# Kernel tuning notes

Measured on AMD Instinct MI355X. Metric: run time of the kernel, lower is better.

## Reference

```python
import jax, jax.numpy as jnp
import numpy as np

D_MODEL = 1024
N_HEADS = 16
D_HEAD = D_MODEL // N_HEADS


def setup_inputs() -> dict:
    key = jax.random.key(0)
    k1, k2, k3 = jax.random.split(key, 3)
    B, N = 2, 2048
    x = jax.random.normal(k1, (B, N, D_MODEL), dtype=jnp.float32)
    # torch nn.Linear(d, 3d, bias=False): y = x @ W.T ; we store W_qkv as [D, 3D]
    scale_in = 1.0 / np.sqrt(D_MODEL)
    W_qkv = jax.random.uniform(k2, (D_MODEL, 3 * D_MODEL), dtype=jnp.float32,
                               minval=-scale_in, maxval=scale_in)
    W_out = jax.random.uniform(k3, (D_MODEL, D_MODEL), dtype=jnp.float32,
                               minval=-scale_in, maxval=scale_in)
    return {"x": x, "W_qkv": W_qkv, "W_out": W_out}


def reference(x, W_qkv, W_out):
    B, N, D = x.shape
    qkv = x @ W_qkv                                    # [B, N, 3D]
    q, k, v = jnp.split(qkv, 3, axis=-1)
    # [B, N, D] -> [B, H, N, d_head]
    def heads(t):
        return t.reshape(B, N, N_HEADS, D_HEAD).transpose(0, 2, 1, 3)
    q, k, v = heads(q), heads(k), heads(v)
    scores = jnp.einsum('bhnd,bhmd->bhnm', q, k) / np.sqrt(D_HEAD)  # [B,H,N,N]
    causal_mask = jnp.triu(jnp.ones((N, N), dtype=bool), k=1)
    scores = jnp.where(causal_mask, -jnp.inf, scores)
    attn = jax.nn.softmax(scores, axis=-1)             # [B,H,N,N]
    out = jnp.einsum('bhnm,bhmd->bhnd', attn, v)       # [B,H,N,d_head]
    out = out.transpose(0, 2, 1, 3).reshape(B, N, D)
    out = out @ W_out.T if False else out @ W_out      # W_out stored [D,D], x @ W
    return out, attn
```

## Files before the change

kernel.cpp:

```cpp
#include <hip/hip_runtime.h>
#include <hip/hip_bf16.h>

typedef __bf16 bf16;
typedef __bf16 bf16x4 __attribute__((ext_vector_type(4)));
typedef __bf16 bf16x8 __attribute__((ext_vector_type(8)));
typedef float  f32x4  __attribute__((ext_vector_type(4)));

#define MFMA16(a, b, c) __builtin_amdgcn_mfma_f32_16x16x32_bf16((a), (b), (c), 0, 0, 0)

typedef const __attribute__((address_space(1))) void* gptr_t;
typedef __attribute__((address_space(3))) void* sptr_t;

__device__ __forceinline__ void load_lds16(const bf16* g, bf16* l) {
  __builtin_amdgcn_global_load_lds((gptr_t)g, (sptr_t)l, 16, 0, 0);
}

__global__ __launch_bounds__(256) void detect_dtype(const unsigned short* __restrict__ w,
                                                    int* __restrict__ flag) {
  __shared__ int cnt[256];
  int c = 0;
#pragma unroll
  for (int k = 0; k < 16; ++k) {
    unsigned short v = w[(threadIdx.x * 16 + k) * 2];
    int e = (v >> 7) & 0xFF;
    c += (e >= 90 && e <= 130) ? 1 : 0;
  }
  cnt[threadIdx.x] = c;
  __syncthreads();
  if (threadIdx.x == 0) {
    int t = 0;
    for (int i = 0; i < 256; ++i) t += cnt[i];
    *flag = (t > 2048) ? 1 : 0;
  }
}

__global__ __launch_bounds__(256) void convert_to_bf16(const void* __restrict__ in,
                                                       bf16* __restrict__ out,
                                                       const int* __restrict__ flag) {
  const int i0 = (blockIdx.x * 256 + threadIdx.x) * 8;
  if (*flag) {
    *(bf16x8*)(out + i0) = *(const bf16x8*)((const bf16*)in + i0);
  } else {
    const float* p = (const float*)in;
    float4 a = *(const float4*)(p + i0);
    float4 b = *(const float4*)(p + i0 + 4);
    bf16x8 v;
    v[0] = (bf16)a.x; v[1] = (bf16)a.y; v[2] = (bf16)a.z; v[3] = (bf16)a.w;
    v[4] = (bf16)b.x; v[5] = (bf16)b.y; v[6] = (bf16)b.z; v[7] = (bf16)b.w;
    *(bf16x8*)(out + i0) = v;
  }
}

__global__ __launch_bounds__(256) void transpose_any(const void* __restrict__ in,
                                                     bf16* __restrict__ out,
                                                     const int* __restrict__ flag,
                                                     int R, int C) {
  __shared__ bf16 t[64][65];
  const int c0 = blockIdx.x * 64, r0 = blockIdx.y * 64;
  const int tid = threadIdx.x;
  const int lc = tid & 63, lr4 = tid >> 6;
  if (*flag) {
    const bf16* p = (const bf16*)in;
#pragma unroll
    for (int i = 0; i < 16; ++i) {
      int r = i * 4 + lr4;
      t[r][lc] = p[(size_t)(r0 + r) * C + c0 + lc];
    }
  } else {
    const float* p = (const float*)in;
#pragma unroll
    for (int i = 0; i < 16; ++i) {
      int r = i * 4 + lr4;
      t[r][lc] = (bf16)p[(size_t)(r0 + r) * C + c0 + lc];
    }
  }
  __syncthreads();
#pragma unroll
  for (int i = 0; i < 16; ++i) {
    int r = i * 4 + lr4;
    out[(size_t)(c0 + r) * R + r0 + lc] = t[lc][r];
  }
}

__global__ __launch_bounds__(256) void transpose_v(const bf16* __restrict__ qkv,
                                                   bf16* __restrict__ vt) {
  __shared__ bf16 t[64][65];
  const int bh = blockIdx.y, b = bh >> 4, h = bh & 15;
  const int j0 = blockIdx.x * 64;
  const int tid = threadIdx.x;
  const int lc = tid & 63, lr4 = tid >> 6;
  const bf16* src = qkv + (size_t)b * 2048 * 3072 + 2048 + (size_t)h * 64;
#pragma unroll
  for (int i = 0; i < 16; ++i) {
    int j = i * 4 + lr4;
    t[j][lc] = src[(size_t)(j0 + j) * 3072 + lc];
  }
  __syncthreads();
  bf16* dst = vt + (size_t)bh * 64 * 2048;
#pragma unroll
  for (int i = 0; i < 16; ++i) {
    int d = i * 4 + lr4;
    dst[(size_t)d * 2048 + j0 + lc] = t[lc][d];
  }
}

template <typename CT>
__global__ __launch_bounds__(256) void gemm_bt(const bf16* __restrict__ A,
                                               const bf16* __restrict__ Bt,
                                               CT* __restrict__ C,
                                               int K, int ldc) {
  __shared__ bf16 a_lds[128 * 32];
  __shared__ bf16 b_lds[128 * 32];
  const int tid = threadIdx.x;
  const int w = tid >> 6, lane = tid & 63, l15 = lane & 15, quad = lane >> 4;
  const int wr = w >> 1, wc = w & 1;
  const int m0 = blockIdx.y * 128, n0 = blockIdx.x * 128;

  const f32x4 fz = {0.f, 0.f, 0.f, 0.f};
  f32x4 acc[4][4];
#pragma unroll
  for (int i = 0; i < 4; ++i)
#pragma unroll
    for (int j = 0; j < 4; ++j) acc[i][j] = fz;

  for (int k0 = 0; k0 < K; k0 += 32) {
#pragma unroll
    for (int i = 0; i < 2; ++i) {
      int c = tid + i * 256;
      int r = c >> 2, kk = c & 3;
      load_lds16(A + (size_t)(m0 + r) * K + k0 + kk * 8, &a_lds[c * 8]);
      load_lds16(Bt + (size_t)(n0 + r) * K + k0 + kk * 8, &b_lds[c * 8]);
    }
    __syncthreads();
    bf16x8 af[4], bfr[4];
#pragma unroll
    for (int mb = 0; mb < 4; ++mb)
      af[mb] = *(const bf16x8*)&a_lds[(wr * 64 + mb * 16 + l15) * 32 + quad * 8];
#pragma unroll
    for (int nb = 0; nb < 4; ++nb)
      bfr[nb] = *(const bf16x8*)&b_lds[(wc * 64 + nb * 16 + l15) * 32 + quad * 8];
#pragma unroll
    for (int mb = 0; mb < 4; ++mb)
#pragma unroll
      for (int nb = 0; nb < 4; ++nb)
        acc[mb][nb] = MFMA16(af[mb], bfr[nb], acc[mb][nb]);
    __syncthreads();
  }

#pragma unroll
  for (int mb = 0; mb < 4; ++mb)
#pragma unroll
    for (int nb = 0; nb < 4; ++nb) {
      int row = m0 + wr * 64 + mb * 16 + quad * 4;
      int col = n0 + wc * 64 + nb * 16 + l15;
#pragma unroll
      for (int r = 0; r < 4; ++r)
        C[(size_t)(row + r) * ldc + col] = (CT)acc[mb][nb][r];
    }
}

__device__ __forceinline__ void compute_st(const bf16* k_lds, const bf16x8 (&qf)[2][2],
                                           int l15, int quad, f32x4 (&st)[8][2]) {
  const f32x4 fz = {0.f, 0.f, 0.f, 0.f};
  __builtin_amdgcn_s_setprio(1);
#pragma unroll
  for (int jb = 0; jb < 8; ++jb) {
    const int jl = jb * 16 + l15;
    const char* kb = (const char*)k_lds + jl * 128;
    const int sw = (jl & 7) << 4;
    bf16x8 kf0 = *(const bf16x8*)(kb + ((quad * 16) ^ sw));
    bf16x8 kf1 = *(const bf16x8*)(kb + ((64 + quad * 16) ^ sw));
    st[jb][0] = MFMA16(kf0, qf[0][0], fz);
    st[jb][0] = MFMA16(kf1, qf[0][1], st[jb][0]);
    st[jb][1] = MFMA16(kf0, qf[1][0], fz);
    st[jb][1] = MFMA16(kf1, qf[1][1], st[jb][1]);
  }
  __builtin_amdgcn_s_setprio(0);
}

__global__ __launch_bounds__(256) void fused_attn(const bf16* __restrict__ qkv,
                                                  const bf16* __restrict__ vt,
                                                  float* __restrict__ attn,
                                                  bf16* __restrict__ o_ws) {
  __shared__ bf16 k_lds[2][128 * 64];
  __shared__ bf16 vt_lds[64 * 128];
  __shared__ bf16 p_lds[128 * 128];

  const int bh = blockIdx.y;
  const int b = bh >> 4, h = bh & 15;
  const int qt = (bh & 16) ? (15 - (int)blockIdx.x) : (int)blockIdx.x;
  const int tid = threadIdx.x;
  const int w = tid >> 6, lane = tid & 63, l15 = lane & 15, quad = lane >> 4;
  const int q0 = qt * 128;

  const char* qkvb = (const char*)qkv;
  const size_t kbyte0 = ((size_t)b * 2048 * 3072 + 1024 + (size_t)h * 64) * 2;
  const size_t vtbyte0 = ((size_t)bh * 64) * 2048 * 2;

  bf16x8 qf[2][2];
#pragma unroll
  for (int ib = 0; ib < 2; ++ib)
#pragma unroll
    for (int ks = 0; ks < 2; ++ks) {
      const bf16* qp = qkv + ((size_t)b * 2048 + q0 + w * 32 + ib * 16 + l15) * 3072
                       + h * 64 + ks * 32 + quad * 8;
      bf16x8 v = *(const bf16x8*)qp;
      bf16x8 sv;
#pragma unroll
      for (int u = 0; u < 8; ++u) sv[u] = (bf16)((float)v[u] * 0.125f);
      qf[ib][ks] = sv;
    }

  float m_run[2] = {-3e38f, -3e38f};
  float l_run[2] = {0.f, 0.f};

  auto stage_k = [&](int kt, int buf) {
#pragma unroll
    for (int c = 0; c < 4; ++c) {
      const int L = c * 4096 + tid * 16;
      const int j = L >> 7, cb = L & 127;
      const char* src = qkvb + kbyte0 + (size_t)(kt * 128 + j) * 6144 + (cb ^ ((j & 7) << 4));
      load_lds16((const bf16*)src, (bf16*)((char*)k_lds[buf] + L));
    }
  };
  auto stage_v = [&](int kt) {
#pragma unroll
    for (int c = 0; c < 4; ++c) {
      const int L = c * 4096 + tid * 16;
      const int d = L >> 8, cb = L & 255;
      const char* src = (const char*)vt + vtbyte0 + (size_t)d * 4096 + kt * 256 + (cb ^ ((d & 7) << 4));
      load_lds16((const bf16*)src, (bf16*)((char*)vt_lds + L));
    }
  };

  stage_k(0, 0);
  __syncthreads();
  for (int kt = 0; kt <= qt; ++kt) {
    if (kt < qt) stage_k(kt + 1, (kt + 1) & 1);

    f32x4 st[8][2];
    compute_st(k_lds[kt & 1], qf, l15, quad, st);

    const bool diag = (kt == qt);
#pragma unroll
    for (int ib = 0; ib < 2; ++ib) {
      const int ig = q0 + w * 32 + ib * 16 + l15;
      float tmax = -3e38f;
#pragma unroll
      for (int jb = 0; jb < 8; ++jb)
#pragma unroll
        for (int r = 0; r < 4; ++r) {
          const int jg = kt * 128 + jb * 16 + quad * 4 + r;
          float s = st[jb][ib][r];
          if (diag && jg > ig) { s = -3e38f; st[jb][ib][r] = s; }
          tmax = fmaxf(tmax, s);
        }
      tmax = fmaxf(tmax, __shfl_xor(tmax, 16));
      tmax = fmaxf(tmax, __shfl_xor(tmax, 32));
      const float mnew = fmaxf(m_run[ib], tmax);
      float tsum = 0.f;
#pragma unroll
      for (int jb = 0; jb < 8; ++jb)
#pragma unroll
        for (int r = 0; r < 4; ++r) {
          const float s = st[jb][ib][r];
          tsum += (s > -1e38f) ? __expf(s - mnew) : 0.f;
        }
      tsum += __shfl_xor(tsum, 16);
      tsum += __shfl_xor(tsum, 32);
      l_run[ib] = l_run[ib] * __expf(m_run[ib] - mnew) + tsum;
      m_run[ib] = mnew;
    }
    __syncthreads();
  }

  const float invl[2] = {1.f / l_run[0], 1.f / l_run[1]};

  f32x4 oacc[2][4];
#pragma unroll
  for (int ib = 0; ib < 2; ++ib)
#pragma unroll
    for (int db = 0; db < 4; ++db) {
      const f32x4 fz = {0.f, 0.f, 0.f, 0.f};
      oacc[ib][db] = fz;
    }

  stage_k(0, 0);
  __syncthreads();
  for (int kt = 0; kt <= qt; ++kt) {
    if (kt < qt) stage_k(kt + 1, (kt + 1) & 1);
    stage_v(kt);

    f32x4 st[8][2];
    compute_st(k_lds[kt & 1], qf, l15, quad, st);

    const bool diag = (kt == qt);
#pragma unroll
    for (int ib = 0; ib < 2; ++ib) {
      const int ig = q0 + w * 32 + ib * 16 + l15;
      const int il = w * 32 + ib * 16 + l15;
#pragma unroll
      for (int jb = 0; jb < 8; ++jb) {
        bf16x4 pk;
#pragma unroll
        for (int r = 0; r < 4; ++r) {
          const int jg = kt * 128 + jb * 16 + quad * 4 + r;
          float p = __expf(st[jb][ib][r] - m_run[ib]) * invl[ib];
          if (diag && jg > ig) p = 0.f;
          pk[r] = (bf16)p;
        }
        *(bf16x4*)((char*)p_lds + il * 256 + ((jb * 32 + quad * 8) ^ ((il & 7) << 4))) = pk;
      }
    }
    __syncthreads();

    {
      float* abase = attn + ((size_t)bh << 22) + (size_t)q0 * 2048 + kt * 128;
#pragma unroll
      for (int it = 0; it < 16; ++it) {
        const int il = it * 8 + w * 2 + (lane >> 5);
        const int jb4 = (lane & 31) * 8;
        bf16x4 pv = *(const bf16x4*)((char*)p_lds + il * 256 + (jb4 ^ ((il & 7) << 4)));
        float4 f = {(float)pv[0], (float)pv[1], (float)pv[2], (float)pv[3]};
        *(float4*)(abase + (size_t)il * 2048 + (lane & 31) * 4) = f;
      }
    }

    __builtin_amdgcn_s_setprio(1);
#pragma unroll
    for (int js = 0; js < 4; ++js) {
      bf16x8 pa[2], vb[4];
#pragma unroll
      for (int ib = 0; ib < 2; ++ib) {
        const int il = w * 32 + ib * 16 + l15;
        pa[ib] = *(const bf16x8*)((char*)p_lds + il * 256 + ((js * 64 + quad * 16) ^ ((il & 7) << 4)));
      }
#pragma unroll
      for (int db = 0; db < 4; ++db) {
        const int dl = db * 16 + l15;
        vb[db] = *(const bf16x8*)((char*)vt_lds + dl * 256 + ((js * 64 + quad * 16) ^ ((dl & 7) << 4)));
      }
#pragma unroll
      for (int ib = 0; ib < 2; ++ib)
#pragma unroll
        for (int db = 0; db < 4; ++db)
          oacc[ib][db] = MFMA16(pa[ib], vb[db], oacc[ib][db]);
    }
    __builtin_amdgcn_s_setprio(0);
    __syncthreads();
  }

  for (int kt = qt + 1; kt < 16; ++kt) {
    float* abase = attn + ((size_t)bh << 22) + (size_t)q0 * 2048 + kt * 128;
    const float4 z4 = {0.f, 0.f, 0.f, 0.f};
#pragma unroll
    for (int it = 0; it < 16; ++it) {
      const int il = it * 8 + w * 2 + (lane >> 5);
      *(float4*)(abase + (size_t)il * 2048 + (lane & 31) * 4) = z4;
    }
  }

#pragma unroll
  for (int ib = 0; ib < 2; ++ib)
#pragma unroll
    for (int db = 0; db < 4; ++db)
#pragma unroll
      for (int r = 0; r < 4; ++r) {
        const int ig = q0 + w * 32 + ib * 16 + quad * 4 + r;
        const int dg = h * 64 + db * 16 + l15;
        o_ws[((size_t)b * 2048 + ig) * 1024 + dg] = (bf16)oacc[ib][db][r];
      }
}

extern "C" void kernel_launch(void* const* d_in, const int* in_sizes, int n_in,
                              void* d_out, int out_size, void* d_ws, size_t ws_size,
                              hipStream_t stream) {
  const void* x_raw = d_in[0];
  const void* w_qkv = d_in[1];
  const void* w_out = d_in[2];
  float* out  = (float*)d_out;
  float* attn = out + 4194304;

  bf16* ws     = (bf16*)d_ws;
  bf16* qkv_ws = ws;
  bf16* x_bf   = ws + 12582912;
  bf16* vt_ws  = ws + 12582912;
  bf16* woT    = ws + 12582912;
  bf16* wqkvT  = ws + 16777216;
  bf16* o_ws   = ws + 16777216;
  int*  flag   = (int*)(ws + 20971520);

  detect_dtype<<<1, 256, 0, stream>>>((const unsigned short*)w_qkv, flag);
  convert_to_bf16<<<2048, 256, 0, stream>>>(x_raw, x_bf, flag);
  transpose_any<<<dim3(48, 16), 256, 0, stream>>>(w_qkv, wqkvT, flag, 1024, 3072);
  gemm_bt<bf16><<<dim3(24, 32), 256, 0, stream>>>(x_bf, wqkvT, qkv_ws, 1024, 3072);
  transpose_v<<<dim3(32, 32), 256, 0, stream>>>(qkv_ws, vt_ws);
  fused_attn<<<dim3(16, 32), 256, 0, stream>>>(qkv_ws, vt_ws, attn, o_ws);
  transpose_any<<<dim3(16, 16), 256, 0, stream>>>(w_out, woT, flag, 1024, 1024);
  gemm_bt<float><<<dim3(8, 32), 256, 0, stream>>>(o_ws, woT, out, 1024, 1024);
}
```

Before: 694.7 us.

## Read K and V fragments directly from global memory, drop LDS staging and barriers

```diff
diff --git a/kernel.cpp b/kernel.cpp
--- a/kernel.cpp
+++ b/kernel.cpp
@@ -159,17 +159,15 @@
     }
 }
 
-__device__ __forceinline__ void compute_st(const bf16* k_lds, const bf16x8 (&qf)[2][2],
-                                           int l15, int quad, f32x4 (&st)[8][2]) {
+__device__ __forceinline__ void qk_tile(const char* kt_base, const bf16x8 (&qf)[2][2],
+                                        int l15, int quad, f32x4 (&st)[8][2]) {
   const f32x4 fz = {0.f, 0.f, 0.f, 0.f};
   __builtin_amdgcn_s_setprio(1);
 #pragma unroll
   for (int jb = 0; jb < 8; ++jb) {
-    const int jl = jb * 16 + l15;
-    const char* kb = (const char*)k_lds + jl * 128;
-    const int sw = (jl & 7) << 4;
-    bf16x8 kf0 = *(const bf16x8*)(kb + ((quad * 16) ^ sw));
-    bf16x8 kf1 = *(const bf16x8*)(kb + ((64 + quad * 16) ^ sw));
+    const char* kr = kt_base + (size_t)(jb * 16 + l15) * 6144 + quad * 16;
+    bf16x8 kf0 = *(const bf16x8*)kr;
+    bf16x8 kf1 = *(const bf16x8*)(kr + 64);
     st[jb][0] = MFMA16(kf0, qf[0][0], fz);
     st[jb][0] = MFMA16(kf1, qf[0][1], st[jb][0]);
     st[jb][1] = MFMA16(kf0, qf[1][0], fz);
@@ -178,12 +176,10 @@
   __builtin_amdgcn_s_setprio(0);
 }
 
-__global__ __launch_bounds__(256) void fused_attn(const bf16* __restrict__ qkv,
-                                                  const bf16* __restrict__ vt,
-                                                  float* __restrict__ attn,
-                                                  bf16* __restrict__ o_ws) {
-  __shared__ bf16 k_lds[2][128 * 64];
-  __shared__ bf16 vt_lds[64 * 128];
+__global__ __launch_bounds__(256, 2) void fused_attn(const bf16* __restrict__ qkv,
+                                                     const bf16* __restrict__ vt,
+                                                     float* __restrict__ attn,
+                                                     bf16* __restrict__ o_ws) {
   __shared__ bf16 p_lds[128 * 128];
 
   const int bh = blockIdx.y;
@@ -195,7 +191,17 @@
 
   const char* qkvb = (const char*)qkv;
   const size_t kbyte0 = ((size_t)b * 2048 * 3072 + 1024 + (size_t)h * 64) * 2;
-  const size_t vtbyte0 = ((size_t)bh * 64) * 2048 * 2;
+  const char* vtb = (const char*)vt + ((size_t)bh * 64) * 2048 * 2;
+
+  for (int kt = qt + 1; kt < 16; ++kt) {
+    float* abase = attn + ((size_t)bh << 22) + (size_t)q0 * 2048 + kt * 128;
+    const f32x4 z4 = {0.f, 0.f, 0.f, 0.f};
+#pragma unroll
+    for (int it = 0; it < 16; ++it) {
+      const int il = it * 8 + w * 2 + (lane >> 5);
+      __builtin_nontemporal_store(z4, (f32x4*)(abase + (size_t)il * 2048 + (lane & 31) * 4));
+    }
+  }
 
   bf16x8 qf[2][2];
 #pragma unroll
@@ -214,32 +220,9 @@
   float m_run[2] = {-3e38f, -3e38f};
   float l_run[2] = {0.f, 0.f};
 
-  auto stage_k = [&](int kt, int buf) {
-#pragma unroll
-    for (int c = 0; c < 4; ++c) {
-      const int L = c * 4096 + tid * 16;
-      const int j = L >> 7, cb = L & 127;
-      const char* src = qkvb + kbyte0 + (size_t)(kt * 128 + j) * 6144 + (cb ^ ((j & 7) << 4));
-      load_lds16((const bf16*)src, (bf16*)((char*)k_lds[buf] + L));
-    }
-  };
-  auto stage_v = [&](int kt) {
-#pragma unroll
-    for (int c = 0; c < 4; ++c) {
-      const int L = c * 4096 + tid * 16;
-      const int d = L >> 8, cb = L & 255;
-      const char* src = (const char*)vt + vtbyte0 + (size_t)d * 4096 + kt * 256 + (cb ^ ((d & 7) << 4));
-      load_lds16((const bf16*)src, (bf16*)((char*)vt_lds + L));
-    }
-  };
-
-  stage_k(0, 0);
-  __syncthreads();
   for (int kt = 0; kt <= qt; ++kt) {
-    if (kt < qt) stage_k(kt + 1, (kt + 1) & 1);
-
     f32x4 st[8][2];
-    compute_st(k_lds[kt & 1], qf, l15, quad, st);
+    qk_tile(qkvb + kbyte0 + (size_t)kt * 128 * 6144, qf, l15, quad, st);
 
     const bool diag = (kt == qt);
 #pragma unroll
@@ -271,7 +254,6 @@
       l_run[ib] = l_run[ib] * __expf(m_run[ib] - mnew) + tsum;
       m_run[ib] = mnew;
     }
-    __syncthreads();
   }
 
   const float invl[2] = {1.f / l_run[0], 1.f / l_run[1]};
@@ -285,14 +267,9 @@
       oacc[ib][db] = fz;
     }
 
-  stage_k(0, 0);
-  __syncthreads();
   for (int kt = 0; kt <= qt; ++kt) {
-    if (kt < qt) stage_k(kt + 1, (kt + 1) & 1);
-    stage_v(kt);
-
     f32x4 st[8][2];
-    compute_st(k_lds[kt & 1], qf, l15, quad, st);
+    qk_tile(qkvb + kbyte0 + (size_t)kt * 128 * 6144, qf, l15, quad, st);
 
     const bool diag = (kt == qt);
 #pragma unroll
@@ -312,52 +289,44 @@
         *(bf16x4*)((char*)p_lds + il * 256 + ((jb * 32 + quad * 8) ^ ((il & 7) << 4))) = pk;
       }
     }
-    __syncthreads();
+
+    bf16x8 vfr[4][4];
+#pragma unroll
+    for (int js = 0; js < 4; ++js)
+#pragma unroll
+      for (int db = 0; db < 4; ++db) {
+        const int dl = db * 16 + l15;
+        vfr[js][db] = *(const bf16x8*)(vtb + (size_t)dl * 4096 + kt * 256 + js * 64 + quad * 16);
+      }
 
     {
       float* abase = attn + ((size_t)bh << 22) + (size_t)q0 * 2048 + kt * 128;
 #pragma unroll
       for (int it = 0; it < 16; ++it) {
-        const int il = it * 8 + w * 2 + (lane >> 5);
+        const int il = w * 32 + it * 2 + (lane >> 5);
         const int jb4 = (lane & 31) * 8;
         bf16x4 pv = *(const bf16x4*)((char*)p_lds + il * 256 + (jb4 ^ ((il & 7) << 4)));
-        float4 f = {(float)pv[0], (float)pv[1], (float)pv[2], (float)pv[3]};
-        *(float4*)(abase + (size_t)il * 2048 + (lane & 31) * 4) = f;
+        f32x4 f = {(float)pv[0], (float)pv[1], (float)pv[2], (float)pv[3]};
+        __builtin_nontemporal_store(f, (f32x4*)(abase + (size_t)il * 2048 + (lane & 31) * 4));
       }
     }
 
     __builtin_amdgcn_s_setprio(1);
 #pragma unroll
     for (int js = 0; js < 4; ++js) {
-      bf16x8 pa[2], vb[4];
+      bf16x8 pa[2];
 #pragma unroll
       for (int ib = 0; ib < 2; ++ib) {
         const int il = w * 32 + ib * 16 + l15;
         pa[ib] = *(const bf16x8*)((char*)p_lds + il * 256 + ((js * 64 + quad * 16) ^ ((il & 7) << 4)));
       }
 #pragma unroll
-      for (int db = 0; db < 4; ++db) {
-        const int dl = db * 16 + l15;
-        vb[db] = *(const bf16x8*)((char*)vt_lds + dl * 256 + ((js * 64 + quad * 16) ^ ((dl & 7) << 4)));
-      }
-#pragma unroll
       for (int ib = 0; ib < 2; ++ib)
 #pragma unroll
         for (int db = 0; db < 4; ++db)
-          oacc[ib][db] = MFMA16(pa[ib], vb[db], oacc[ib][db]);
+          oacc[ib][db] = MFMA16(pa[ib], vfr[js][db], oacc[ib][db]);
     }
     __builtin_amdgcn_s_setprio(0);
-    __syncthreads();
-  }
-
-  for (int kt = qt + 1; kt < 16; ++kt) {
-    float* abase = attn + ((size_t)bh << 22) + (size_t)q0 * 2048 + kt * 128;
-    const float4 z4 = {0.f, 0.f, 0.f, 0.f};
-#pragma unroll
-    for (int it = 0; it < 16; ++it) {
-      const int il = it * 8 + w * 2 + (lane >> 5);
-      *(float4*)(abase + (size_t)il * 2048 + (lane & 31) * 4) = z4;
-    }
   }
 
 #pragma unroll
```

After: 743.7 us. 7.1% more time.
